# Kernel optimization log

Hardware: AMD Instinct MI355X
Metric: run time of the kernel (lower is better)

Reference implementation:

```python
import jax, jax.numpy as jnp
import numpy as np

NUM_EXPERTS = 64


def setup_inputs() -> dict:
    key = jax.random.key(0)
    k1, k2 = jax.random.split(key)
    num_tokens, d_model, top_k = 32768, 1024, 2
    hidden_states = jax.random.normal(k1, (num_tokens, d_model), dtype=jnp.float32)
    routing_indices = jax.random.randint(k2, (num_tokens, top_k), 0, NUM_EXPERTS, dtype=jnp.int64)
    return {"hidden_states": hidden_states, "routing_indices": routing_indices}


def reference(hidden_states, routing_indices):
    """Single-EP-rank (expert_parallel_size==1) AllToAllDispatcher.permute.

    Math: bincount tokens per expert; stable-sort flattened top-k routing
    indices by expert; gather (duplicate) tokens into expert-sorted order.
    With ep_size==1 the all-to-all is the identity, and the post-dispatch
    expert sort (argsort of the already-sorted routing indices) is computed
    exactly as in the original code.
    """
    num_tokens, top_k = routing_indices.shape
    flat = routing_indices.reshape(-1)  # [num_tokens * top_k]

    # torch.bincount(routing_indices.flatten(), minlength=num_experts)
    num_tokens_per_expert = jnp.bincount(flat, length=NUM_EXPERTS)

    # ops.permute: stable sort by expert id, replicate tokens top_k times
    sorted_idx = jnp.argsort(flat)  # stable by default in jax
    inverse_permute_mapping = sorted_idx
    permuted = hidden_states[sorted_idx // top_k]  # [num_tokens*top_k, d_model]

    # ep_size == 1: all_to_all is identity; dispatched routing indices are the
    # sorted flattened routing indices (contributions.sort() in source)
    dispatched_routing = jnp.sort(flat)
    expert_sort_indices = jnp.argsort(dispatched_routing)  # stable
    sorted_and_dispatched = permuted[expert_sort_indices]

    num_local_dispatched_tokens_per_expert = jnp.bincount(
        dispatched_routing.astype(jnp.int32), length=NUM_EXPERTS
    )
    return (
        sorted_and_dispatched,
        inverse_permute_mapping,
        expert_sort_indices,
        num_local_dispatched_tokens_per_expert,
    )
```

## Files before the change

kernel.cpp:

```cpp
#include <hip/hip_runtime.h>

#define NEXP  64
#define NTOK  32768
#define TOPK  2
#define NFLAT (NTOK * TOPK)
#define DM    1024
#define NBLK  256
#define EPB   (NFLAT / NBLK)
#define DETBLK 64

typedef float v4f __attribute__((ext_vector_type(4)));

#define O1 ((size_t)NFLAT * DM)
#define O2 (O1 + NFLAT)
#define O3 (O2 + NFLAT)

#define WS_DET 0
#define WS_BC  (WS_DET + DETBLK)

__global__ void k_detect(const int4* __restrict__ routing4, int* __restrict__ ws) {
    __shared__ int o;
    int t = threadIdx.x;
    if (t == 0) o = 0;
    __syncthreads();
    int k = blockIdx.x * 256 + t;
    int4 w = routing4[k];
    int acc = w.y | w.w;
    if (__any(acc != 0)) { if ((t & 63) == 0) atomicOr(&o, 1); }
    __syncthreads();
    if (t == 0) ws[WS_DET + blockIdx.x] = o;
}

__device__ __forceinline__ int get_stride(const int* ws) {
    __shared__ int strideSh;
    int t = threadIdx.x;
    if (t < 64) {
        int v = ws[WS_DET + t];
        unsigned long long b = __ballot(v != 0);
        if (t == 0) strideSh = b ? 1 : 2;
    }
    __syncthreads();
    return strideSh;
}

__global__ void k_hist(const int* __restrict__ routing, int* __restrict__ ws) {
    __shared__ int h[NEXP];
    int t = threadIdx.x;
    const int stride = get_stride(ws);
    if (t < NEXP) h[t] = 0;
    __syncthreads();
    int i = blockIdx.x * EPB + t;
    int e = routing[(size_t)i * stride];
    atomicAdd(&h[e], 1);
    __syncthreads();
    if (t < NEXP) ws[WS_BC + blockIdx.x * NEXP + t] = h[t];
}

__global__ void __launch_bounds__(512)
k_main(const int* __restrict__ routing, const int* __restrict__ ws,
       const float* __restrict__ hidden, float* __restrict__ out) {
    __shared__ int se[EPB];
    __shared__ int dstSh[EPB];
    __shared__ int s1h[4][NEXP], s2h[4][NEXP];
    __shared__ int boSh[NEXP];
    const int t = threadIdx.x;
    const int b = blockIdx.x;
    const int stride = get_stride(ws);

    if (t < EPB) {
        int i = b * EPB + t;
        se[t] = routing[(size_t)i * stride];
    }
    if (t < 256) {
        int e = t & 63, c = t >> 6;
        int s1 = 0, s2 = 0;
        #pragma unroll 8
        for (int r = c * 64; r < c * 64 + 64; ++r) {
            int v = ws[WS_BC + r * NEXP + e];
            s2 += v;
            s1 += (r < b) ? v : 0;
        }
        s1h[c][e] = s1; s2h[c][e] = s2;
    }
    __syncthreads();
    if (t < 64) {
        int e = t;
        int pre = s1h[0][e] + s1h[1][e] + s1h[2][e] + s1h[3][e];
        int tot = s2h[0][e] + s2h[1][e] + s2h[2][e] + s2h[3][e];
        int x = tot;
        #pragma unroll
        for (int d = 1; d < 64; d <<= 1) {
            int y = __shfl_up(x, d, 64);
            if (e >= d) x += y;
        }
        boSh[e] = (x - tot) + pre;
        if (b == 0) out[O3 + e] = (float)tot;
    }
    __syncthreads();
    if (t < 256) {
        int e = se[t];
        int rank = 0;
        for (int j = 0; j < t; ++j) rank += (se[j] == e) ? 1 : 0;
        int dst = boSh[e] + rank;
        dstSh[t] = dst;
        int i = b * EPB + t;
        out[O1 + dst] = (float)i;
        out[O2 + i] = (float)i;
    }
    __syncthreads();
    const int half = t >> 8;
    const int lt = t & 255;
    #pragma unroll 4
    for (int k = 0; k < 128; k += 2) {
        int tokLocal = k + half;
        int tok = b * 128 + tokLocal;
        const v4f* src = (const v4f*)(hidden + (size_t)tok * DM);
        v4f v = src[lt];
        int d0 = dstSh[2 * tokLocal];
        int d1 = dstSh[2 * tokLocal + 1];
        __builtin_nontemporal_store(v, (v4f*)(out + (size_t)d0 * DM) + lt);
        __builtin_nontemporal_store(v, (v4f*)(out + (size_t)d1 * DM) + lt);
    }
}

extern "C" void kernel_launch(void* const* d_in, const int* in_sizes, int n_in,
                              void* d_out, int out_size, void* d_ws, size_t ws_size,
                              hipStream_t stream) {
    const float* hidden = (const float*)d_in[0];
    const int* routing = (const int*)d_in[1];
    float* out = (float*)d_out;
    int* ws = (int*)d_ws;

    k_detect<<<DETBLK, 256, 0, stream>>>((const int4*)routing, ws);
    k_hist<<<NBLK, EPB, 0, stream>>>(routing, ws);
    k_main<<<NBLK, 512, 0, stream>>>(routing, ws, hidden, out);
}
```

Measured before the change: 76.89 us.

## Fuse detect, histogram and scatter kernels into one with grid barriers

Merges the three launches (int64 layout detection, per-block histogram, main scatter/copy) into a single persistent kernel of 256 blocks. Two atomic-counter grid barriers replace the kernel boundaries, and a memset resets the counters. This removes two launch gaps and re-reading of routing data, at the risk of deadlock if not all 256 blocks are co-resident, plus spin-wait overhead.

```diff
diff --git a/kernel.cpp b/kernel.cpp
--- a/kernel.cpp
+++ b/kernel.cpp
@@ -7,7 +7,6 @@
 #define DM    1024
 #define NBLK  256
 #define EPB   (NFLAT / NBLK)
-#define DETBLK 64
 
 typedef float v4f __attribute__((ext_vector_type(4)));
 
@@ -15,62 +14,61 @@
 #define O2 (O1 + NFLAT)
 #define O3 (O2 + NFLAT)
 
-#define WS_DET 0
-#define WS_BC  (WS_DET + DETBLK)
+#define WS_CNT 0
+#define WS_DET 8
+#define WS_BC  (WS_DET + NBLK)
 
-__global__ void k_detect(const int4* __restrict__ routing4, int* __restrict__ ws) {
-    __shared__ int o;
-    int t = threadIdx.x;
-    if (t == 0) o = 0;
+__device__ __forceinline__ void gbar(int* cnt) {
     __syncthreads();
-    int k = blockIdx.x * 256 + t;
-    int4 w = routing4[k];
-    int acc = w.y | w.w;
-    if (__any(acc != 0)) { if ((t & 63) == 0) atomicOr(&o, 1); }
-    __syncthreads();
-    if (t == 0) ws[WS_DET + blockIdx.x] = o;
-}
-
-__device__ __forceinline__ int get_stride(const int* ws) {
-    __shared__ int strideSh;
-    int t = threadIdx.x;
-    if (t < 64) {
-        int v = ws[WS_DET + t];
-        unsigned long long b = __ballot(v != 0);
-        if (t == 0) strideSh = b ? 1 : 2;
+    if (threadIdx.x == 0) {
+        __threadfence();
+        atomicAdd(cnt, 1);
+        while (atomicAdd(cnt, 0) < NBLK) __builtin_amdgcn_s_sleep(1);
+        __threadfence();
     }
     __syncthreads();
-    return strideSh;
-}
-
-__global__ void k_hist(const int* __restrict__ routing, int* __restrict__ ws) {
-    __shared__ int h[NEXP];
-    int t = threadIdx.x;
-    const int stride = get_stride(ws);
-    if (t < NEXP) h[t] = 0;
-    __syncthreads();
-    int i = blockIdx.x * EPB + t;
-    int e = routing[(size_t)i * stride];
-    atomicAdd(&h[e], 1);
-    __syncthreads();
-    if (t < NEXP) ws[WS_BC + blockIdx.x * NEXP + t] = h[t];
 }
 
 __global__ void __launch_bounds__(512)
-k_main(const int* __restrict__ routing, const int* __restrict__ ws,
-       const float* __restrict__ hidden, float* __restrict__ out) {
+k_all(const int* __restrict__ routing, int* __restrict__ ws,
+      const float* __restrict__ hidden, float* __restrict__ out) {
     __shared__ int se[EPB];
     __shared__ int dstSh[EPB];
     __shared__ int s1h[4][NEXP], s2h[4][NEXP];
     __shared__ int boSh[NEXP];
+    __shared__ int h[NEXP];
+    __shared__ int flagSh;
     const int t = threadIdx.x;
     const int b = blockIdx.x;
-    const int stride = get_stride(ws);
+
+    int w = 0;
+    if (t < EPB) { w = routing[b * EPB + t]; se[t] = w; }
+    unsigned long long ball = __ballot((t < EPB) && (t & 1) && (w != 0));
+    if (t == 0) flagSh = 0;
+    __syncthreads();
+    if ((t & 63) == 0 && ball) atomicOr(&flagSh, 1);
+    __syncthreads();
+    if (t == 0) ws[WS_DET + b] = flagSh;
+
+    gbar(&ws[WS_CNT + 0]);
+
+    if (t == 0) flagSh = 0;
+    __syncthreads();
+    if (t < NBLK && ws[WS_DET + t] != 0) atomicOr(&flagSh, 1);
+    if (t < NEXP) h[t] = 0;
+    __syncthreads();
+    const int stride = flagSh ? 1 : 2;
 
     if (t < EPB) {
-        int i = b * EPB + t;
-        se[t] = routing[(size_t)i * stride];
+        int e = (stride == 1) ? se[t] : routing[(size_t)(b * EPB + t) * 2];
+        se[t] = e;
+        atomicAdd(&h[e], 1);
     }
+    __syncthreads();
+    if (t < NEXP) ws[WS_BC + b * NEXP + t] = h[t];
+
+    gbar(&ws[WS_CNT + 1]);
+
     if (t < 256) {
         int e = t & 63, c = t >> 6;
         int s1 = 0, s2 = 0;
@@ -97,7 +95,8 @@
         if (b == 0) out[O3 + e] = (float)tot;
     }
     __syncthreads();
-    if (t < 256) {
+
+    if (t < EPB) {
         int e = se[t];
         int rank = 0;
         for (int j = 0; j < t; ++j) rank += (se[j] == e) ? 1 : 0;
@@ -108,6 +107,7 @@
         out[O2 + i] = (float)i;
     }
     __syncthreads();
+
     const int half = t >> 8;
     const int lt = t & 255;
     #pragma unroll 4
@@ -131,7 +131,6 @@
     float* out = (float*)d_out;
     int* ws = (int*)d_ws;
 
-    k_detect<<<DETBLK, 256, 0, stream>>>((const int4*)routing, ws);
-    k_hist<<<NBLK, EPB, 0, stream>>>(routing, ws);
-    k_main<<<NBLK, 512, 0, stream>>>(routing, ws, hidden, out);
+    hipMemsetAsync(ws + WS_CNT, 0, 2 * sizeof(int), stream);
+    k_all<<<NBLK, 512, 0, stream>>>(routing, ws, hidden, out);
 }
```

Result: slower. 103.9 us (+35.2%).

## Reorder copy loop by destination so output rows are written contiguously per expert

Applied to the files above, without the earlier changes.

Each block now computes a local expert-sorted order of its flat entries, using a second prefix scan over the block's own histogram. The copy loop then iterates over destination rows in expert-sorted order, which makes consecutive stores contiguous within each expert's segment. Before, it read each token once and wrote it to two scattered rows. Each source row is now read twice instead of once, trading extra (likely cached) reads for more sequential write patterns.

```diff
diff --git a/kernel.cpp b/kernel.cpp
--- a/kernel.cpp
+++ b/kernel.cpp
@@ -61,8 +61,9 @@
        const float* __restrict__ hidden, float* __restrict__ out) {
     __shared__ int se[EPB];
     __shared__ int dstSh[EPB];
+    __shared__ int orderSh[EPB];
     __shared__ int s1h[4][NEXP], s2h[4][NEXP];
-    __shared__ int boSh[NEXP];
+    __shared__ int boSh[NEXP], loSh[NEXP];
     const int t = threadIdx.x;
     const int b = blockIdx.x;
     const int stride = get_stride(ws);
@@ -87,22 +88,26 @@
         int e = t;
         int pre = s1h[0][e] + s1h[1][e] + s1h[2][e] + s1h[3][e];
         int tot = s2h[0][e] + s2h[1][e] + s2h[2][e] + s2h[3][e];
-        int x = tot;
+        int hb = ws[WS_BC + b * NEXP + e];
+        int x = tot, y = hb;
         #pragma unroll
         for (int d = 1; d < 64; d <<= 1) {
-            int y = __shfl_up(x, d, 64);
-            if (e >= d) x += y;
+            int xx = __shfl_up(x, d, 64);
+            int yy = __shfl_up(y, d, 64);
+            if (e >= d) { x += xx; y += yy; }
         }
         boSh[e] = (x - tot) + pre;
+        loSh[e] = y - hb;
         if (b == 0) out[O3 + e] = (float)tot;
     }
     __syncthreads();
-    if (t < 256) {
+    if (t < EPB) {
         int e = se[t];
         int rank = 0;
         for (int j = 0; j < t; ++j) rank += (se[j] == e) ? 1 : 0;
         int dst = boSh[e] + rank;
         dstSh[t] = dst;
+        orderSh[loSh[e] + rank] = t;
         int i = b * EPB + t;
         out[O1 + dst] = (float)i;
         out[O2 + i] = (float)i;
@@ -110,16 +115,15 @@
     __syncthreads();
     const int half = t >> 8;
     const int lt = t & 255;
-    #pragma unroll 4
-    for (int k = 0; k < 128; k += 2) {
-        int tokLocal = k + half;
-        int tok = b * 128 + tokLocal;
-        const v4f* src = (const v4f*)(hidden + (size_t)tok * DM);
+    #pragma unroll 2
+    for (int p = 0; p < EPB; p += 2) {
+        int pe = p + half;
+        int ts = orderSh[pe];
+        int srcTok = (b * EPB + ts) >> 1;
+        const v4f* src = (const v4f*)(hidden + (size_t)srcTok * DM);
         v4f v = src[lt];
-        int d0 = dstSh[2 * tokLocal];
-        int d1 = dstSh[2 * tokLocal + 1];
-        __builtin_nontemporal_store(v, (v4f*)(out + (size_t)d0 * DM) + lt);
-        __builtin_nontemporal_store(v, (v4f*)(out + (size_t)d1 * DM) + lt);
+        int d = dstSh[ts];
+        __builtin_nontemporal_store(v, (v4f*)(out + (size_t)d * DM) + lt);
     }
 }
 
```

New measurement: 91.96 us. +19.6%, slower.
